# Kernel tuning notes

Hardware: AMD Instinct MI355X
Metric: run time of the kernel (lower is better)

Reference implementation:

```python
import jax, jax.numpy as jnp
import numpy as np

B, T, C = 2, 2048, 1024
NUM_HEADS, NUM_KV_HEADS, HEAD_DIM = 16, 8, 64
R = NUM_HEADS // NUM_KV_HEADS  # q heads per kv head
WINDOW = 512
HIDDEN = 4096
SOFT_CAP = 50.0


def setup_inputs() -> dict:
    key = jax.random.key(0)
    ks = jax.random.split(key, 10)
    std = 0.02
    return {
        "x": jax.random.normal(ks[0], (B, T, C), jnp.float32),
        "kurtosis_sum": jnp.zeros((), jnp.float32),
        "rms1_scale": jnp.zeros((C,), jnp.float32),
        "q_kernel": std * jax.random.normal(ks[1], (C, R, NUM_KV_HEADS, HEAD_DIM), jnp.float32),
        "k_kernel": std * jax.random.normal(ks[2], (C, NUM_KV_HEADS, HEAD_DIM), jnp.float32),
        "v_kernel": std * jax.random.normal(ks[3], (C, NUM_KV_HEADS, HEAD_DIM), jnp.float32),
        "out_kernel": std * jax.random.normal(ks[4], (R, NUM_KV_HEADS, HEAD_DIM, C), jnp.float32),
        "rms2_scale": jnp.zeros((C,), jnp.float32),
        "gate_kernel": std * jax.random.normal(ks[5], (C, HIDDEN), jnp.float32),
        "up_kernel": std * jax.random.normal(ks[6], (C, HIDDEN), jnp.float32),
        "down_kernel": std * jax.random.normal(ks[7], (HIDDEN, C), jnp.float32),
    }


def sine_table(features, length, max_timescale=1e6):
    fraction = jnp.arange(0, features, 2, dtype=jnp.float32) / features
    rot_freq = 1.0 / (max_timescale ** fraction)
    sinusoid = jnp.arange(length, dtype=jnp.float32)[:, None] * rot_freq[None, :]
    sinusoid = jnp.concatenate([sinusoid, sinusoid], axis=-1)  # (T, features)
    return jnp.sin(sinusoid), jnp.cos(sinusoid)


def rotate_half(x):
    x1, x2 = jnp.split(x, 2, axis=-1)
    return jnp.concatenate([-x2, x1], axis=-1)


def rms_norm(x, scale):
    var = jnp.mean(jnp.square(x.astype(jnp.float32)), axis=-1, keepdims=True)
    normed = (x * jax.lax.rsqrt(var + 1e-6)).astype(x.dtype)
    return normed * (1 + scale)


def excess_kurtosis(emb):
    mean = jnp.mean(emb, axis=-1, keepdims=True)
    std = jnp.std(emb, axis=-1, keepdims=True)
    centralized = emb - mean
    fourth = jnp.mean(centralized ** 4, axis=-1, keepdims=True)
    kurt = jnp.squeeze(fourth / (std ** 4 + 1e-6), axis=-1).reshape(-1) - 3
    return jnp.sum(jnp.maximum(kurt, 0.0))


def reference(x, kurtosis_sum, rms1_scale, q_kernel, k_kernel, v_kernel,
              out_kernel, rms2_scale, gate_kernel, up_kernel, down_kernel):
    Bc, Tc, Cc = x.shape
    # sliding-window causal mask: j <= i and |i - j| < WINDOW
    idx = jnp.arange(Tc)
    causal = idx[:, None] >= idx[None, :]
    band = jnp.abs(idx[:, None] - idx[None, :]) < WINDOW
    mask = (causal & band)[None, None, None]  # (1,1,1,T,T) for brhsd scores

    # --- attention ---
    attn_in = rms_norm(x, rms1_scale)
    q = jnp.einsum('bsm,mrhk->brhsk', attn_in, q_kernel)
    k = jnp.einsum('bdm,mhk->bhdk', attn_in, k_kernel)
    v = jnp.einsum('bdm,mhv->bhdv', attn_in, v_kernel)

    sin, cos = sine_table(HEAD_DIM, Tc, max_timescale=1e6)
    q = q * cos[None, None, None] + rotate_half(q) * sin[None, None, None]
    k = k * cos[None, None] + rotate_half(k) * sin[None, None]

    scale = jax.lax.rsqrt(jnp.asarray(HEAD_DIM, dtype=x.dtype))
    qk = jnp.einsum('brhsk,bhdk->brhsd', q, k) * scale
    qk = jnp.tanh(qk / SOFT_CAP) * SOFT_CAP
    probs = jax.nn.softmax(qk.astype(jnp.float32), where=mask).astype(x.dtype)
    qkv = jnp.einsum('brhsd,bhdv->brhsv', probs, v)
    attn_out = jnp.einsum('brhsv,rhvm->bsm', qkv, out_kernel)
    x = x + attn_out

    # --- SwiGLU MLP ---
    mlp_in = rms_norm(x, rms2_scale)
    gate = jax.nn.silu(mlp_in @ gate_kernel)
    up = mlp_in @ up_kernel
    x = x + (up * gate) @ down_kernel

    return (x, kurtosis_sum + excess_kurtosis(x))
```

## Files before the change

kernel.cpp:

```cpp
#include <hip/hip_runtime.h>
#include <hip/hip_bf16.h>

typedef __attribute__((ext_vector_type(8))) short short8;
typedef __attribute__((ext_vector_type(4))) float f32x4;
typedef __attribute__((ext_vector_type(4))) int int4v;
typedef __attribute__((ext_vector_type(8))) int int8v;

#define DEVFN static __device__ __forceinline__

DEVFN float bf2f(unsigned short u) {
    unsigned int i = ((unsigned int)u) << 16;
    float f; __builtin_memcpy(&f, &i, 4); return f;
}
DEVFN unsigned short f2bf(float f) {
    unsigned int i; __builtin_memcpy(&i, &f, 4);
    unsigned int r = i + 0x7fffu + ((i >> 16) & 1u);
    return (unsigned short)(r >> 16);
}
DEVFN unsigned char f2fp8(float f) {
    int r = __builtin_amdgcn_cvt_pk_fp8_f32(f, f, 0, false);
    return (unsigned char)(r & 0xff);
}

DEVFN void load_lds16(const void* g, void* l) {
    __builtin_amdgcn_global_load_lds(
        (__attribute__((address_space(1))) void*)g,
        (__attribute__((address_space(3))) void*)l, 16, 0, 0);
}

DEVFN f32x4 mfma_fp8(int8v a, int8v b, f32x4 c) {
    return __builtin_amdgcn_mfma_scale_f32_16x16x128_f8f6f4(
        a, b, c, 0, 0, 0, 0x7F7F7F7F, 0, 0x7F7F7F7F);
}

constexpr int Bsz = 2, T = 2048, C = 1024;
constexpr int NH = 16, NKV = 8, HD = 64;
constexpr int HID = 4096;
constexpr int NTOK = Bsz * T;
constexpr size_t MiB = 1024 * 1024;

constexpr size_t OFF_WQKV = 0;
constexpr size_t OFF_WOUT = 4 * MiB;
constexpr size_t OFF_WGATE = 6 * MiB;
constexpr size_t OFF_WUP = 10 * MiB;
constexpr size_t OFF_WDOWN = 14 * MiB;
constexpr size_t OFF_XN1 = 18 * MiB;
constexpr size_t OFF_QKVP = 26 * MiB;
constexpr size_t OFF_P2 = 26 * MiB;
constexpr size_t OFF_QB = 58 * MiB;
constexpr size_t OFF_KB = 66 * MiB;
constexpr size_t OFF_VT = 70 * MiB;
constexpr size_t OFF_CTX = 74 * MiB;
constexpr size_t OFF_X2 = 82 * MiB;
constexpr size_t OFF_XN2 = 98 * MiB;
constexpr size_t OFF_G = 102 * MiB;
constexpr size_t OFF_P4 = 118 * MiB;

__global__ __launch_bounds__(256) void prep_kernel(
    const float* __restrict__ qk, const float* __restrict__ kk2,
    const float* __restrict__ vk, const float* __restrict__ ok,
    const float* __restrict__ gk, const float* __restrict__ uk,
    const float* __restrict__ dk,
    unsigned short* __restrict__ wqkv, unsigned short* __restrict__ wout,
    unsigned char* __restrict__ wgate, unsigned char* __restrict__ wup,
    unsigned char* __restrict__ wdown,
    const float* __restrict__ x, const float* __restrict__ rms1_scale,
    unsigned short* __restrict__ xn1) {
    __shared__ float t[32][33];
    __shared__ float red[4];
    int id = blockIdx.x;
    int tid = threadIdx.x;
    if (id >= 15360) {
        int row = id - 15360;
        const float4 v = *(const float4*)&x[(size_t)row * 1024 + tid * 4];
        float ss = v.x * v.x + v.y * v.y + v.z * v.z + v.w * v.w;
#pragma unroll
        for (int m = 32; m; m >>= 1) ss += __shfl_xor(ss, m, 64);
        if ((tid & 63) == 0) red[tid >> 6] = ss;
        __syncthreads();
        float tot = red[0] + red[1] + red[2] + red[3];
        float inv = rsqrtf(tot * (1.f / 1024.f) + 1e-6f);
        const float4 sc = *(const float4*)&rms1_scale[tid * 4];
        size_t o = (size_t)row * 1024 + tid * 4;
        xn1[o + 0] = f2bf(v.x * inv * (1.f + sc.x));
        xn1[o + 1] = f2bf(v.y * inv * (1.f + sc.y));
        xn1[o + 2] = f2bf(v.z * inv * (1.f + sc.z));
        xn1[o + 3] = f2bf(v.w * inv * (1.f + sc.w));
        return;
    }
    const float* in; int K, N, nx, base; int fp8 = 0;
    unsigned short* out16 = nullptr; unsigned char* out8 = nullptr;
    if (id < 1024)       { in = qk;  out16 = wqkv;                       K = 1024; N = 1024; nx = 32;  base = 0; }
    else if (id < 1536)  { in = kk2; out16 = wqkv + (size_t)1024 * 1024; K = 1024; N = 512;  nx = 16;  base = 1024; }
    else if (id < 2048)  { in = vk;  out16 = wqkv + (size_t)1536 * 1024; K = 1024; N = 512;  nx = 16;  base = 1536; }
    else if (id < 3072)  { in = ok;  out16 = wout;                       K = 1024; N = 1024; nx = 32;  base = 2048; }
    else if (id < 7168)  { in = gk;  out8 = wgate; fp8 = 1;              K = 1024; N = 4096; nx = 128; base = 3072; }
    else if (id < 11264) { in = uk;  out8 = wup; fp8 = 1;                K = 1024; N = 4096; nx = 128; base = 7168; }
    else                 { in = dk;  out8 = wdown; fp8 = 1;              K = 4096; N = 1024; nx = 32;  base = 11264; }
    int lid = id - base;
    int n0 = (lid % nx) * 32, k0 = (lid / nx) * 32;
    int tx = tid & 31, ty = tid >> 5;
#pragma unroll
    for (int i = 0; i < 4; i++)
        t[ty + 8 * i][tx] = in[(size_t)(k0 + ty + 8 * i) * N + n0 + tx];
    __syncthreads();
    if (fp8) {
#pragma unroll
        for (int i = 0; i < 4; i++)
            out8[(size_t)(n0 + ty + 8 * i) * K + k0 + tx] = f2fp8(t[tx][ty + 8 * i] * 16.f);
    } else {
#pragma unroll
        for (int i = 0; i < 4; i++)
            out16[(size_t)(n0 + ty + 8 * i) * K + k0 + tx] = f2bf(t[tx][ty + 8 * i]);
    }
}

__global__ __launch_bounds__(256) void gemm128(const unsigned short* __restrict__ A,
                                               const unsigned short* __restrict__ Bt,
                                               unsigned short* __restrict__ Cp,
                                               int N, int K, int lda, int ldb,
                                               size_t zA, size_t zB, size_t zC) {
    __shared__ __align__(16) unsigned short As[128 * 32];
    __shared__ __align__(16) unsigned short Bs[128 * 32];
    A += (size_t)blockIdx.z * zA;
    Bt += (size_t)blockIdx.z * zB;
    const int tid = threadIdx.x;
    const int lane = tid & 63, w = tid >> 6;
    const int quad = lane >> 4, l15 = lane & 15;
    const int wr = w >> 1, wc = w & 1;
    const int m0 = blockIdx.y * 128, n0 = blockIdx.x * 128;

    f32x4 acc[4][4];
#pragma unroll
    for (int i = 0; i < 4; i++)
#pragma unroll
        for (int j = 0; j < 4; j++) acc[i][j] = f32x4{0.f, 0.f, 0.f, 0.f};

    const int stRow = (w << 4) + (lane >> 2);
    const int stCol = (lane & 3) << 3;

    for (int kk = 0; kk < K; kk += 32) {
#pragma unroll
        for (int i = 0; i < 2; i++) {
            load_lds16(A + (size_t)(m0 + (i << 6) + stRow) * lda + kk + stCol,
                       &As[((i << 6) + (w << 4)) * 32]);
            load_lds16(Bt + (size_t)(n0 + (i << 6) + stRow) * ldb + kk + stCol,
                       &Bs[((i << 6) + (w << 4)) * 32]);
        }
        __syncthreads();
        short8 a[4], b[4];
#pragma unroll
        for (int mi = 0; mi < 4; mi++)
            a[mi] = *(const short8*)&As[(wr * 64 + mi * 16 + l15) * 32 + quad * 8];
#pragma unroll
        for (int ni = 0; ni < 4; ni++)
            b[ni] = *(const short8*)&Bs[(wc * 64 + ni * 16 + l15) * 32 + quad * 8];
#pragma unroll
        for (int mi = 0; mi < 4; mi++)
#pragma unroll
            for (int ni = 0; ni < 4; ni++)
                acc[mi][ni] = __builtin_amdgcn_mfma_f32_16x16x32_bf16(a[mi], b[ni], acc[mi][ni], 0, 0, 0);
        __syncthreads();
    }
#pragma unroll
    for (int mi = 0; mi < 4; mi++)
#pragma unroll
        for (int ni = 0; ni < 4; ni++)
#pragma unroll
            for (int r = 0; r < 4; r++) {
                int row = m0 + wr * 64 + mi * 16 + quad * 4 + r;
                int col = n0 + wc * 64 + ni * 16 + l15;
                Cp[(size_t)blockIdx.z * zC + (size_t)row * N + col] = f2bf(acc[mi][ni][r]);
            }
}

DEVFN int8v read_frag8(const unsigned char* buf, int rb, int quad) {
    int base = rb * 128;
    int h0 = (2 * quad) ^ (rb & 7);
    int h1 = (2 * quad + 1) ^ (rb & 7);
    int4v lo = *(const int4v*)&buf[base + h0 * 16];
    int4v hi = *(const int4v*)&buf[base + h1 * 16];
    return int8v{lo.x, lo.y, lo.z, lo.w, hi.x, hi.y, hi.z, hi.w};
}

__global__ __launch_bounds__(256) void gateup_kernel(const unsigned char* __restrict__ A,
                                                     const unsigned char* __restrict__ Bg,
                                                     const unsigned char* __restrict__ Bu,
                                                     unsigned char* __restrict__ out) {
    __shared__ __align__(16) unsigned char As[128 * 128];
    __shared__ __align__(16) unsigned char Gs[64 * 128];
    __shared__ __align__(16) unsigned char Us[64 * 128];
    const int tid = threadIdx.x;
    const int lane = tid & 63, w = tid >> 6;
    const int quad = lane >> 4, l15 = lane & 15;
    const int wr = w >> 1, wc = w & 1;
    const int m0 = blockIdx.y * 128, n0 = blockIdx.x * 64;

    f32x4 aG[4][2], aU[4][2];
#pragma unroll
    for (int i = 0; i < 4; i++)
#pragma unroll
        for (int j = 0; j < 2; j++) { aG[i][j] = f32x4{0.f, 0.f, 0.f, 0.f}; aU[i][j] = f32x4{0.f, 0.f, 0.f, 0.f}; }

    const int lrow = lane >> 3;
    const int hA = (lane & 7) ^ lrow;

    for (int kk = 0; kk < 1024; kk += 128) {
#pragma unroll
        for (int j = 0; j < 4; j++) {
            int i = w * 4 + j;
            int r = i * 8 + lrow;
            load_lds16(A + (size_t)(m0 + r) * 1024 + kk + hA * 16, &As[i * 1024]);
        }
#pragma unroll
        for (int j = 0; j < 2; j++) {
            int i = w * 2 + j;
            int r = i * 8 + lrow;
            load_lds16(Bg + (size_t)(n0 + r) * 1024 + kk + hA * 16, &Gs[i * 1024]);
            load_lds16(Bu + (size_t)(n0 + r) * 1024 + kk + hA * 16, &Us[i * 1024]);
        }
        __syncthreads();
        int8v a[4], bg[2], bu[2];
#pragma unroll
        for (int mi = 0; mi < 4; mi++)
            a[mi] = read_frag8(As, wr * 64 + mi * 16 + l15, quad);
#pragma unroll
        for (int ni = 0; ni < 2; ni++) {
            bg[ni] = read_frag8(Gs, wc * 32 + ni * 16 + l15, quad);
            bu[ni] = read_frag8(Us, wc * 32 + ni * 16 + l15, quad);
        }
#pragma unroll
        for (int mi = 0; mi < 4; mi++)
#pragma unroll
            for (int ni = 0; ni < 2; ni++) {
                aG[mi][ni] = mfma_fp8(a[mi], bg[ni], aG[mi][ni]);
                aU[mi][ni] = mfma_fp8(a[mi], bu[ni], aU[mi][ni]);
            }
        __syncthreads();
    }
#pragma unroll
    for (int mi = 0; mi < 4; mi++)
#pragma unroll
        for (int ni = 0; ni < 2; ni++)
#pragma unroll
            for (int r = 0; r < 4; r++) {
                int row = m0 + wr * 64 + mi * 16 + quad * 4 + r;
                int col = n0 + wc * 32 + ni * 16 + l15;
                float vg = aG[mi][ni][r] * (1.f / 64.f);
                float vu = aU[mi][ni][r] * (1.f / 64.f);
                float s = vg / (1.f + __expf(-vg));
                out[(size_t)row * 4096 + col] = f2fp8(s * vu * 8.f);
            }
}

__global__ __launch_bounds__(256) void down_gemm(const unsigned char* __restrict__ A,
                                                 const unsigned char* __restrict__ Bt,
                                                 unsigned short* __restrict__ Cp) {
    __shared__ __align__(16) unsigned char As[128 * 128];
    __shared__ __align__(16) unsigned char Bs[128 * 128];
    const int tid = threadIdx.x;
    const int lane = tid & 63, w = tid >> 6;
    const int quad = lane >> 4, l15 = lane & 15;
    const int wr = w >> 1, wc = w & 1;
    const int m0 = blockIdx.y * 128, n0 = blockIdx.x * 128;
    const int kbase = blockIdx.z * 1024;

    f32x4 acc[4][4];
#pragma unroll
    for (int i = 0; i < 4; i++)
#pragma unroll
        for (int j = 0; j < 4; j++) acc[i][j] = f32x4{0.f, 0.f, 0.f, 0.f};

    const int lrow = lane >> 3;
    const int hA = (lane & 7) ^ lrow;

    for (int kk = 0; kk < 1024; kk += 128) {
#pragma unroll
        for (int j = 0; j < 4; j++) {
            int i = w * 4 + j;
            int r = i * 8 + lrow;
            load_lds16(A + (size_t)(m0 + r) * 4096 + kbase + kk + hA * 16, &As[i * 1024]);
            load_lds16(Bt + (size_t)(n0 + r) * 4096 + kbase + kk + hA * 16, &Bs[i * 1024]);
        }
        __syncthreads();
        int8v a[4], b[4];
#pragma unroll
        for (int mi = 0; mi < 4; mi++)
            a[mi] = read_frag8(As, wr * 64 + mi * 16 + l15, quad);
#pragma unroll
        for (int ni = 0; ni < 4; ni++)
            b[ni] = read_frag8(Bs, wc * 64 + ni * 16 + l15, quad);
#pragma unroll
        for (int mi = 0; mi < 4; mi++)
#pragma unroll
            for (int ni = 0; ni < 4; ni++)
                acc[mi][ni] = mfma_fp8(a[mi], b[ni], acc[mi][ni]);
        __syncthreads();
    }
    const size_t Z = (size_t)NTOK * 1024;
#pragma unroll
    for (int mi = 0; mi < 4; mi++)
#pragma unroll
        for (int ni = 0; ni < 4; ni++)
#pragma unroll
            for (int r = 0; r < 4; r++) {
                int row = m0 + wr * 64 + mi * 16 + quad * 4 + r;
                int col = n0 + wc * 64 + ni * 16 + l15;
                Cp[(size_t)blockIdx.z * Z + (size_t)row * 1024 + col] =
                    f2bf(acc[mi][ni][r] * (1.f / 128.f));
            }
}

__global__ __launch_bounds__(256) void reduce_out(const unsigned short* __restrict__ p,
                                                  const float* __restrict__ x,
                                                  const float* __restrict__ scale,
                                                  float* __restrict__ x2,
                                                  unsigned char* __restrict__ xn2,
                                                  const float* __restrict__ ksum,
                                                  float* __restrict__ outk) {
    __shared__ float red[4];
    int row = blockIdx.x, tid = threadIdx.x;
    if (row == 0 && tid == 0) outk[0] = ksum[0];
    size_t base = (size_t)row * 1024 + tid * 4;
    const size_t Z = (size_t)NTOK * 1024;
    float4 v = *(const float4*)&x[base];
#pragma unroll
    for (int z = 0; z < 4; z++) {
        ushort4 u = *(const ushort4*)&p[base + z * Z];
        v.x += bf2f(u.x); v.y += bf2f(u.y); v.z += bf2f(u.z); v.w += bf2f(u.w);
    }
    *(float4*)&x2[base] = v;
    float ss = v.x * v.x + v.y * v.y + v.z * v.z + v.w * v.w;
#pragma unroll
    for (int m = 32; m; m >>= 1) ss += __shfl_xor(ss, m, 64);
    if ((tid & 63) == 0) red[tid >> 6] = ss;
    __syncthreads();
    float tot = red[0] + red[1] + red[2] + red[3];
    float inv = rsqrtf(tot * (1.f / 1024.f) + 1e-6f) * 4.f;
    const float4 sc = *(const float4*)&scale[tid * 4];
    xn2[base + 0] = f2fp8(v.x * inv * (1.f + sc.x));
    xn2[base + 1] = f2fp8(v.y * inv * (1.f + sc.y));
    xn2[base + 2] = f2fp8(v.z * inv * (1.f + sc.z));
    xn2[base + 3] = f2fp8(v.w * inv * (1.f + sc.w));
}

__global__ __launch_bounds__(256) void reduce_down(const unsigned short* __restrict__ p,
                                                   const float* __restrict__ x2,
                                                   float* __restrict__ outx,
                                                   float* __restrict__ outk) {
    __shared__ float red[4], r2[4], r4[4];
    int row = blockIdx.x, tid = threadIdx.x;
    size_t base = (size_t)row * 1024 + tid * 4;
    const size_t Z = (size_t)NTOK * 1024;
    float4 v = *(const float4*)&x2[base];
#pragma unroll
    for (int z = 0; z < 4; z++) {
        ushort4 u = *(const ushort4*)&p[base + z * Z];
        v.x += bf2f(u.x); v.y += bf2f(u.y); v.z += bf2f(u.z); v.w += bf2f(u.w);
    }
    *(float4*)&outx[base] = v;
    float s = v.x + v.y + v.z + v.w;
#pragma unroll
    for (int m = 32; m; m >>= 1) s += __shfl_xor(s, m, 64);
    if ((tid & 63) == 0) red[tid >> 6] = s;
    __syncthreads();
    float mean = (red[0] + red[1] + red[2] + red[3]) * (1.f / 1024.f);
    float cx = v.x - mean, cy = v.y - mean, cz = v.z - mean, cw = v.w - mean;
    float x2v = cx * cx, y2 = cy * cy, z2 = cz * cz, w2 = cw * cw;
    float c2 = x2v + y2 + z2 + w2;
    float c4 = x2v * x2v + y2 * y2 + z2 * z2 + w2 * w2;
#pragma unroll
    for (int m = 32; m; m >>= 1) {
        c2 += __shfl_xor(c2, m, 64);
        c4 += __shfl_xor(c4, m, 64);
    }
    if ((tid & 63) == 0) { r2[tid >> 6] = c2; r4[tid >> 6] = c4; }
    __syncthreads();
    if (tid == 0) {
        float m2 = (r2[0] + r2[1] + r2[2] + r2[3]) * (1.f / 1024.f);
        float m4 = (r4[0] + r4[1] + r4[2] + r4[3]) * (1.f / 1024.f);
        float kurt = m4 / (m2 * m2 + 1e-6f) - 3.f;
        if (kurt > 0.f) atomicAdd(outk, kurt);
    }
}

__global__ __launch_bounds__(256) void ropevt_kernel(const unsigned short* __restrict__ qkvp,
                                                     unsigned short* __restrict__ qb,
                                                     unsigned short* __restrict__ kb,
                                                     unsigned short* __restrict__ vt) {
    __shared__ float sv[32], cv[32];
    __shared__ unsigned short tile[64][68];
    const size_t Z = (size_t)NTOK * 2048;
    int id = blockIdx.x;
    int tid = threadIdx.x;
    if (id < NTOK) {
        int tok = id;
        int b = tok >> 11, t = tok & 2047;
        if (tid < 32) {
            float fr = (float)tid * (1.f / 32.f);
            float freq = powf(1e6f, -fr);
            float a = (float)t * freq;
            sv[tid] = sinf(a);
            cv[tid] = cosf(a);
        }
        __syncthreads();
        const unsigned short* r0 = qkvp + (size_t)tok * 2048;
        const unsigned short* r1 = r0 + Z;
#pragma unroll
        for (int e = tid; e < 1536; e += 256) {
            int u = e >> 6, d = e & 63;
            int col = (u < 16) ? (u * 64 + d) : (1024 + (u - 16) * 64 + d);
            int pcol = (d < 32) ? col + 32 : col - 32;
            float sgn = (d < 32) ? -1.f : 1.f;
            float vc = bf2f(r0[col]) + bf2f(r1[col]);
            float vp = bf2f(r0[pcol]) + bf2f(r1[pcol]);
            float o = vc * cv[d & 31] + sgn * vp * sv[d & 31];
            if (u < 16)
                qb[((size_t)(b * 16 + u) * 2048 + t) * 64 + d] = f2bf(o);
            else
                kb[((size_t)(b * 8 + (u - 16)) * 2048 + t) * 64 + d] = f2bf(o);
        }
    } else {
        int lid = id - NTOK;
        int b = lid >> 8, h = (lid >> 5) & 7, t0 = (lid & 31) * 64;
        int d = tid & 63, tr = tid >> 6;
#pragma unroll
        for (int i = 0; i < 16; i++) {
            int t = tr + i * 4;
            size_t gi = (size_t)(b * 2048 + t0 + t) * 2048 + 1536 + h * 64 + d;
            tile[t][d] = f2bf(bf2f(qkvp[gi]) + bf2f(qkvp[gi + Z]));
        }
        __syncthreads();
        int tt = tid & 63, dr = tid >> 6;
#pragma unroll
        for (int i = 0; i < 16; i++) {
            int dd = dr + i * 4;
            vt[((size_t)(b * 8 + h) * 64 + dd) * 2048 + t0 + tt] = tile[tt][dd];
        }
    }
}

__global__ __launch_bounds__(256) void attn_kernel(const unsigned short* __restrict__ qb,
                                                   const unsigned short* __restrict__ kb,
                                                   const unsigned short* __restrict__ vt,
                                                   unsigned short* __restrict__ ctx) {
    __shared__ __align__(16) unsigned short P[4][16 * 32];
    const int tid = threadIdx.x, lane = tid & 63, w = tid >> 6;
    const int quad = lane >> 4, l15 = lane & 15;
    const int qt = blockIdx.x, H = blockIdx.y, b = blockIdx.z;
    const int hkv = H & 7;
    const int qw = qt * 64 + w * 16;

    const unsigned short* qbase = qb + ((size_t)(b * 16 + H) * 2048 + qw) * 64;
    short8 aq0 = *(const short8*)(qbase + (size_t)l15 * 64 + quad * 8);
    short8 aq1 = *(const short8*)(qbase + (size_t)l15 * 64 + 32 + quad * 8);

    const unsigned short* kbase = kb + (size_t)(b * 8 + hkv) * 2048 * 64;
    const unsigned short* vbase = vt + (size_t)(b * 8 + hkv) * 64 * 2048;

    f32x4 O[4];
#pragma unroll
    for (int i = 0; i < 4; i++) O[i] = f32x4{0.f, 0.f, 0.f, 0.f};
    float lrow[4] = {0.f, 0.f, 0.f, 0.f};

    int kstart = qw - 511;
    if (kstart < 0) kstart = 0;
    kstart &= ~31;
    unsigned short* Pw = P[w];

    for (int k0 = kstart; k0 <= qw + 15; k0 += 32) {
        f32x4 S[2];
#pragma unroll
        for (int c = 0; c < 2; c++) {
            const unsigned short* kp = kbase + (size_t)(k0 + c * 16 + l15) * 64 + quad * 8;
            short8 kf0 = *(const short8*)kp;
            short8 kf1 = *(const short8*)(kp + 32);
            f32x4 s = __builtin_amdgcn_mfma_f32_16x16x32_bf16(aq0, kf0, f32x4{0.f, 0.f, 0.f, 0.f}, 0, 0, 0);
            s = __builtin_amdgcn_mfma_f32_16x16x32_bf16(aq1, kf1, s, 0, 0, 0);
            S[c] = s;
        }
        float p[2][4];
#pragma unroll
        for (int c = 0; c < 2; c++)
#pragma unroll
            for (int r = 0; r < 4; r++) {
                int i = qw + quad * 4 + r;
                int j = k0 + c * 16 + l15;
                float tt = S[c][r] * (0.125f * 0.02f);
                tt = fminf(8.f, fmaxf(-8.f, tt));
                float e = __expf(2.f * tt);
                float y = 50.f * (e - 1.f) / (e + 1.f);
                bool ok = (j <= i) && ((i - j) < 512);
                p[c][r] = ok ? __expf(y) : 0.f;
            }
#pragma unroll
        for (int r = 0; r < 4; r++) {
            float rs = p[0][r] + p[1][r];
#pragma unroll
            for (int mm = 8; mm; mm >>= 1) rs += __shfl_xor(rs, mm, 16);
            lrow[r] += rs;
        }
#pragma unroll
        for (int c = 0; c < 2; c++)
#pragma unroll
            for (int r = 0; r < 4; r++)
                Pw[(quad * 4 + r) * 32 + c * 16 + l15] = f2bf(p[c][r]);
        asm volatile("s_waitcnt lgkmcnt(0)" ::: "memory");
        short8 pf = *(const short8*)&Pw[l15 * 32 + quad * 8];
#pragma unroll
        for (int ni = 0; ni < 4; ni++) {
            short8 vf = *(const short8*)(vbase + (size_t)(ni * 16 + l15) * 2048 + k0 + quad * 8);
            O[ni] = __builtin_amdgcn_mfma_f32_16x16x32_bf16(pf, vf, O[ni], 0, 0, 0);
        }
        asm volatile("s_waitcnt lgkmcnt(0)" ::: "memory");
    }
#pragma unroll
    for (int r = 0; r < 4; r++) {
        float inv = 1.f / lrow[r];
        int i = qw + quad * 4 + r;
        size_t tok = (size_t)b * 2048 + i;
#pragma unroll
        for (int ni = 0; ni < 4; ni++)
            ctx[tok * 1024 + H * 64 + ni * 16 + l15] = f2bf(O[ni][r] * inv);
    }
}

extern "C" void kernel_launch(void* const* d_in, const int* in_sizes, int n_in,
                              void* d_out, int out_size, void* d_ws, size_t ws_size,
                              hipStream_t stream) {
    const float* x = (const float*)d_in[0];
    const float* ksum = (const float*)d_in[1];
    const float* rms1_scale = (const float*)d_in[2];
    const float* q_w = (const float*)d_in[3];
    const float* k_w = (const float*)d_in[4];
    const float* v_w = (const float*)d_in[5];
    const float* out_w = (const float*)d_in[6];
    const float* rms2_scale = (const float*)d_in[7];
    const float* gate_w = (const float*)d_in[8];
    const float* up_w = (const float*)d_in[9];
    const float* down_w = (const float*)d_in[10];

    char* ws = (char*)d_ws;
    unsigned short* wqkv = (unsigned short*)(ws + OFF_WQKV);
    unsigned short* wout = (unsigned short*)(ws + OFF_WOUT);
    unsigned char* wgate = (unsigned char*)(ws + OFF_WGATE);
    unsigned char* wup = (unsigned char*)(ws + OFF_WUP);
    unsigned char* wdown = (unsigned char*)(ws + OFF_WDOWN);
    unsigned short* xn1 = (unsigned short*)(ws + OFF_XN1);
    unsigned short* qkvp = (unsigned short*)(ws + OFF_QKVP);
    unsigned short* p2 = (unsigned short*)(ws + OFF_P2);
    unsigned short* qb = (unsigned short*)(ws + OFF_QB);
    unsigned short* kb = (unsigned short*)(ws + OFF_KB);
    unsigned short* vtb = (unsigned short*)(ws + OFF_VT);
    unsigned short* ctx = (unsigned short*)(ws + OFF_CTX);
    float* x2 = (float*)(ws + OFF_X2);
    unsigned char* xn2 = (unsigned char*)(ws + OFF_XN2);
    unsigned char* g = (unsigned char*)(ws + OFF_G);
    unsigned short* p4 = (unsigned short*)(ws + OFF_P4);
    float* outx = (float*)d_out;
    float* outk = outx + (size_t)NTOK * C;

    prep_kernel<<<15360 + NTOK, 256, 0, stream>>>(
        q_w, k_w, v_w, out_w, gate_w, up_w, down_w,
        wqkv, wout, wgate, wup, wdown, x, rms1_scale, xn1);

    gemm128<<<dim3(2048 / 128, NTOK / 128, 2), 256, 0, stream>>>(
        xn1, wqkv, qkvp, 2048, 512, 1024, 1024, 512, 512, (size_t)NTOK * 2048);

    ropevt_kernel<<<NTOK + 512, 256, 0, stream>>>(qkvp, qb, kb, vtb);

    attn_kernel<<<dim3(T / 64, NH, Bsz), 256, 0, stream>>>(qb, kb, vtb, ctx);

    gemm128<<<dim3(1024 / 128, NTOK / 128, 4), 256, 0, stream>>>(
        ctx, wout, p2, 1024, 256, 1024, 1024, 256, 256, (size_t)NTOK * 1024);
    reduce_out<<<NTOK, 256, 0, stream>>>(p2, x, rms2_scale, x2, xn2, ksum, outk);

    gateup_kernel<<<dim3(HID / 64, NTOK / 128), 256, 0, stream>>>(xn2, wgate, wup, g);

    down_gemm<<<dim3(1024 / 128, NTOK / 128, 4), 256, 0, stream>>>(g, wdown, p4);
    reduce_down<<<NTOK, 256, 0, stream>>>(p4, x2, outx, outk);

    (void)in_sizes; (void)n_in; (void)out_size; (void)ws_size;
}
```

Measured before the change: 385.7 us.

## Widen attention key tiles to 64, compute row sums via MFMA, use fast reciprocals

The attention loop now processes 64 keys per iteration instead of 32 and double-buffers the per-wave P tile in LDS, which removes the second lgkmcnt wait. Row sums of the softmax probabilities are computed by an MFMA against a ones vector instead of shuffle reductions, and the tanh soft-cap is rewritten as 50 - 100/(e+1) using a hardware reciprocal. The SwiGLU epilogue also swaps a division for the fast reciprocal. The row sums now come from bf16-rounded probabilities and the reciprocal is approximate, which slightly changes numerics. The wider tile also computes more fully masked entries near the window edges.

```diff
diff --git a/kernel.cpp b/kernel.cpp
--- a/kernel.cpp
+++ b/kernel.cpp
@@ -21,6 +21,7 @@
     int r = __builtin_amdgcn_cvt_pk_fp8_f32(f, f, 0, false);
     return (unsigned char)(r & 0xff);
 }
+DEVFN float fastrcp(float x) { return __builtin_amdgcn_rcpf(x); }
 
 DEVFN void load_lds16(const void* g, void* l) {
     __builtin_amdgcn_global_load_lds(
@@ -248,7 +249,7 @@
                 int col = n0 + wc * 32 + ni * 16 + l15;
                 float vg = aG[mi][ni][r] * (1.f / 64.f);
                 float vu = aU[mi][ni][r] * (1.f / 64.f);
-                float s = vg / (1.f + __expf(-vg));
+                float s = vg * fastrcp(1.f + __expf(-vg));
                 out[(size_t)row * 4096 + col] = f2fp8(s * vu * 8.f);
             }
 }
@@ -444,7 +445,7 @@
                                                    const unsigned short* __restrict__ kb,
                                                    const unsigned short* __restrict__ vt,
                                                    unsigned short* __restrict__ ctx) {
-    __shared__ __align__(16) unsigned short P[4][16 * 32];
+    __shared__ __align__(16) unsigned short P[4][2][16 * 64];
     const int tid = threadIdx.x, lane = tid & 63, w = tid >> 6;
     const int quad = lane >> 4, l15 = lane & 15;
     const int qt = blockIdx.x, H = blockIdx.y, b = blockIdx.z;
@@ -458,20 +459,23 @@
     const unsigned short* kbase = kb + (size_t)(b * 8 + hkv) * 2048 * 64;
     const unsigned short* vbase = vt + (size_t)(b * 8 + hkv) * 64 * 2048;
 
+    const short bf1 = (short)0x3F80;
+    const short8 ones = {bf1, bf1, bf1, bf1, bf1, bf1, bf1, bf1};
+
     f32x4 O[4];
 #pragma unroll
     for (int i = 0; i < 4; i++) O[i] = f32x4{0.f, 0.f, 0.f, 0.f};
-    float lrow[4] = {0.f, 0.f, 0.f, 0.f};
+    f32x4 lacc = f32x4{0.f, 0.f, 0.f, 0.f};
 
     int kstart = qw - 511;
     if (kstart < 0) kstart = 0;
-    kstart &= ~31;
-    unsigned short* Pw = P[w];
-
-    for (int k0 = kstart; k0 <= qw + 15; k0 += 32) {
-        f32x4 S[2];
-#pragma unroll
-        for (int c = 0; c < 2; c++) {
+    kstart &= ~63;
+    int buf = 0;
+
+    for (int k0 = kstart; k0 <= qw + 15; k0 += 64) {
+        f32x4 S[4];
+#pragma unroll
+        for (int c = 0; c < 4; c++) {
             const unsigned short* kp = kbase + (size_t)(k0 + c * 16 + l15) * 64 + quad * 8;
             short8 kf0 = *(const short8*)kp;
             short8 kf1 = *(const short8*)(kp + 32);
@@ -479,44 +483,38 @@
             s = __builtin_amdgcn_mfma_f32_16x16x32_bf16(aq1, kf1, s, 0, 0, 0);
             S[c] = s;
         }
-        float p[2][4];
-#pragma unroll
-        for (int c = 0; c < 2; c++)
+        unsigned short* Pw = P[w][buf];
+#pragma unroll
+        for (int c = 0; c < 4; c++)
 #pragma unroll
             for (int r = 0; r < 4; r++) {
                 int i = qw + quad * 4 + r;
                 int j = k0 + c * 16 + l15;
-                float tt = S[c][r] * (0.125f * 0.02f);
-                tt = fminf(8.f, fmaxf(-8.f, tt));
-                float e = __expf(2.f * tt);
-                float y = 50.f * (e - 1.f) / (e + 1.f);
+                float Sc = fminf(3200.f, fmaxf(-3200.f, S[c][r]));
+                float e = __expf(Sc * 0.005f);
+                float y = 50.f - 100.f * fastrcp(e + 1.f);
                 bool ok = (j <= i) && ((i - j) < 512);
-                p[c][r] = ok ? __expf(y) : 0.f;
+                float pv = ok ? __expf(y) : 0.f;
+                Pw[(quad * 4 + r) * 64 + c * 16 + l15] = f2bf(pv);
             }
-#pragma unroll
-        for (int r = 0; r < 4; r++) {
-            float rs = p[0][r] + p[1][r];
-#pragma unroll
-            for (int mm = 8; mm; mm >>= 1) rs += __shfl_xor(rs, mm, 16);
-            lrow[r] += rs;
-        }
-#pragma unroll
-        for (int c = 0; c < 2; c++)
-#pragma unroll
-            for (int r = 0; r < 4; r++)
-                Pw[(quad * 4 + r) * 32 + c * 16 + l15] = f2bf(p[c][r]);
         asm volatile("s_waitcnt lgkmcnt(0)" ::: "memory");
-        short8 pf = *(const short8*)&Pw[l15 * 32 + quad * 8];
+        short8 pf0 = *(const short8*)&Pw[l15 * 64 + quad * 8];
+        short8 pf1 = *(const short8*)&Pw[l15 * 64 + 32 + quad * 8];
 #pragma unroll
         for (int ni = 0; ni < 4; ni++) {
-            short8 vf = *(const short8*)(vbase + (size_t)(ni * 16 + l15) * 2048 + k0 + quad * 8);
-            O[ni] = __builtin_amdgcn_mfma_f32_16x16x32_bf16(pf, vf, O[ni], 0, 0, 0);
-        }
-        asm volatile("s_waitcnt lgkmcnt(0)" ::: "memory");
+            const unsigned short* vp = vbase + (size_t)(ni * 16 + l15) * 2048 + k0;
+            short8 vf0 = *(const short8*)(vp + quad * 8);
+            short8 vf1 = *(const short8*)(vp + 32 + quad * 8);
+            O[ni] = __builtin_amdgcn_mfma_f32_16x16x32_bf16(pf0, vf0, O[ni], 0, 0, 0);
+            O[ni] = __builtin_amdgcn_mfma_f32_16x16x32_bf16(pf1, vf1, O[ni], 0, 0, 0);
+        }
+        lacc = __builtin_amdgcn_mfma_f32_16x16x32_bf16(pf0, ones, lacc, 0, 0, 0);
+        lacc = __builtin_amdgcn_mfma_f32_16x16x32_bf16(pf1, ones, lacc, 0, 0, 0);
+        buf ^= 1;
     }
 #pragma unroll
     for (int r = 0; r < 4; r++) {
-        float inv = 1.f / lrow[r];
+        float inv = fastrcp(lacc[r]);
         int i = qw + quad * 4 + r;
         size_t tok = (size_t)b * 2048 + i;
 #pragma unroll
```

Measured after the change: 379.3 us. No clear change (-1.7%).
